# Kernel tuning notes

Hardware: AMD Instinct MI355X
Metric: run time of the kernel (lower is better)

The kernel has to match this reference:

```python
import jax, jax.numpy as jnp
import numpy as np

T, H, E, I = 512, 2048, 8, 1024


def setup_inputs() -> dict:
    key = jax.random.key(0)
    k1, k2, k3, k4 = jax.random.split(key, 4)
    x = jax.random.normal(k1, (T, H), dtype=jnp.float32)
    router_logits = jax.random.normal(k2, (T, E), dtype=jnp.float32)
    # w13 stacks [gate; up] along the output dim: [E, 2I, H]
    w13_weight = jax.random.normal(k3, (E, 2 * I, H), dtype=jnp.float32) * (1.0 / np.sqrt(H))
    w2_weight = jax.random.normal(k4, (E, H, I), dtype=jnp.float32) * (1.0 / np.sqrt(I))
    return {"x": x, "router_logits": router_logits, "w13_weight": w13_weight,
            "w2_weight": w2_weight, "top_k": 2}


def reference(x, router_logits, w13_weight, w2_weight, top_k):
    t, h = x.shape
    e = router_logits.shape[-1]
    # select_experts: softmax -> top_k -> renormalize
    probs = jax.nn.softmax(router_logits.astype(jnp.float32), axis=-1)  # [T, E]
    topk_w, topk_ids = jax.lax.top_k(probs, top_k)                      # [T, K]
    topk_w = topk_w / jnp.sum(topk_w, axis=-1, keepdims=True)
    # dense combine weights [T, E]; zero for unselected experts
    combine = jnp.zeros((t, e), dtype=x.dtype).at[
        jnp.arange(t)[:, None], topk_ids
    ].add(topk_w.astype(x.dtype))
    # grouped expert SwiGLU MLP (computed densely over experts, masked by combine)
    gu = jnp.einsum('th,enh->ten', x, w13_weight)   # [T, E, 2I]
    i = gu.shape[-1] // 2
    gate, up = gu[..., :i], gu[..., i:]
    act = jax.nn.silu(gate) * up                    # [T, E, I]
    y = jnp.einsum('tei,ehi->teh', act, w2_weight)  # [T, E, H]
    return jnp.einsum('teh,te->th', y, combine)     # weighted combine [T, H]
```

## Files before the change

### kernel.cpp

```cpp
#include <hip/hip_runtime.h>
#include <hip/hip_bf16.h>

#define T_TOK 512
#define H_DIM 2048
#define E_NUM 8
#define I_DIM 1024

typedef __attribute__((ext_vector_type(8))) short short8;
typedef __attribute__((ext_vector_type(4))) float f32x4;

__device__ __forceinline__ unsigned short f2bf(float f) {
    unsigned int u = __float_as_uint(f);
    u += 0x7fff + ((u >> 16) & 1);
    return (unsigned short)(u >> 16);
}

__device__ __forceinline__ short8 pack8(float4 a, float4 b) {
    short8 r;
    r[0] = (short)f2bf(a.x); r[1] = (short)f2bf(a.y);
    r[2] = (short)f2bf(a.z); r[3] = (short)f2bf(a.w);
    r[4] = (short)f2bf(b.x); r[5] = (short)f2bf(b.y);
    r[6] = (short)f2bf(b.z); r[7] = (short)f2bf(b.w);
    return r;
}

__device__ __forceinline__ short8 cvt8(float4 a, float4 b) {
    union { short8 s; __hip_bfloat162 h[4]; } u;
    u.h[0] = __float22bfloat162_rn(make_float2(a.x, a.y));
    u.h[1] = __float22bfloat162_rn(make_float2(a.z, a.w));
    u.h[2] = __float22bfloat162_rn(make_float2(b.x, b.y));
    u.h[3] = __float22bfloat162_rn(make_float2(b.z, b.w));
    return u.s;
}

__device__ __forceinline__ void gload_lds16(const float* g, float* l) {
    __builtin_amdgcn_global_load_lds(
        (const __attribute__((address_space(1))) void*)g,
        (__attribute__((address_space(3))) void*)l, 16, 0, 0);
}

__global__ __launch_bounds__(512) void routing_kernel(
    const float* __restrict__ logits,
    int* __restrict__ count, int* __restrict__ bucket,
    float* __restrict__ pair_w)
{
    int t = threadIdx.x;
    if (t < E_NUM) count[t] = 0;
    __syncthreads();

    float p[E_NUM];
    float m = -INFINITY;
#pragma unroll
    for (int e = 0; e < E_NUM; ++e) {
        p[e] = logits[t * E_NUM + e];
        m = fmaxf(m, p[e]);
    }
#pragma unroll
    for (int e = 0; e < E_NUM; ++e) p[e] = expf(p[e] - m);
    int i0 = 0;
#pragma unroll
    for (int e = 1; e < E_NUM; ++e) if (p[e] > p[i0]) i0 = e;
    int i1 = (i0 == 0) ? 1 : 0;
#pragma unroll
    for (int e = 0; e < E_NUM; ++e) if (e != i0 && p[e] > p[i1]) i1 = e;
    float denom = p[i0] + p[i1];
    pair_w[2 * t + 0] = p[i0] / denom;
    pair_w[2 * t + 1] = p[i1] / denom;

    int pos0 = atomicAdd(&count[i0], 1);
    bucket[i0 * T_TOK + pos0] = 2 * t + 0;
    int pos1 = atomicAdd(&count[i1], 1);
    bucket[i1 * T_TOK + pos1] = 2 * t + 1;
}

__global__ __launch_bounds__(256) void gemm1_silu_kernel(
    const float* __restrict__ x, const float* __restrict__ w13,
    const int* __restrict__ count, const int* __restrict__ bucket,
    __hip_bfloat16* __restrict__ act)
{
    const int e   = blockIdx.z;
    const int n_e = count[e];
    const int m0  = blockIdx.y * 64;
    if (m0 >= n_e) return;
    const int n0  = blockIdx.x * 64;

    __shared__ float lds[3 * 64 * 64];
    float* sA = lds;
    float* sG = lds + 4096;
    float* sU = lds + 8192;

    const int tid  = threadIdx.x;
    const int lane = tid & 63;
    const int wid  = tid >> 6;
    const int fr   = lane & 15;
    const int fq   = lane >> 4;
    const int wr   = wid >> 1;
    const int wc   = wid & 1;

    const int lrow = lane >> 4;
    const int slot = lane & 15;

    const float* aptr[4];
    const float* gptr[4];
    const float* uptr[4];
#pragma unroll
    for (int i = 0; i < 4; ++i) {
        int r   = 16 * wid + 4 * i + lrow;
        int gsl = slot ^ (r & 7);
        int arow = min(m0 + r, n_e - 1);
        int tok  = bucket[e * T_TOK + arow] >> 1;
        aptr[i] = x + (size_t)tok * H_DIM + gsl * 4;
        gptr[i] = w13 + ((size_t)e * (2 * I_DIM) + n0 + r) * H_DIM + gsl * 4;
        uptr[i] = w13 + ((size_t)e * (2 * I_DIM) + I_DIM + n0 + r) * H_DIM + gsl * 4;
    }

    f32x4 accg[2][2] = {};
    f32x4 accu[2][2] = {};

#pragma unroll
    for (int i = 0; i < 4; ++i) {
        float* dA = &sA[(16 * wid + 4 * i) * 64];
        float* dG = &sG[(16 * wid + 4 * i) * 64];
        float* dU = &sU[(16 * wid + 4 * i) * 64];
        gload_lds16(aptr[i], dA);
        gload_lds16(gptr[i], dG);
        gload_lds16(uptr[i], dU);
    }

    for (int kb = 64; kb <= H_DIM; kb += 64) {
        __syncthreads();

        short8 a[2][2], bg[2][2], bu[2][2];
#pragma unroll
        for (int kk = 0; kk < 2; ++kk) {
#pragma unroll
            for (int m = 0; m < 2; ++m) {
                int r  = wr * 32 + m * 16 + fr;
                int s0 = (kk * 8 + fq * 2) ^ (r & 7);
                float4 q0 = *(const float4*)&sA[r * 64 + s0 * 4];
                float4 q1 = *(const float4*)&sA[r * 64 + (s0 ^ 1) * 4];
                a[kk][m] = cvt8(q0, q1);
            }
#pragma unroll
            for (int n = 0; n < 2; ++n) {
                int r  = wc * 32 + n * 16 + fr;
                int s0 = (kk * 8 + fq * 2) ^ (r & 7);
                float4 g0 = *(const float4*)&sG[r * 64 + s0 * 4];
                float4 g1 = *(const float4*)&sG[r * 64 + (s0 ^ 1) * 4];
                bg[kk][n] = cvt8(g0, g1);
                float4 u0 = *(const float4*)&sU[r * 64 + s0 * 4];
                float4 u1 = *(const float4*)&sU[r * 64 + (s0 ^ 1) * 4];
                bu[kk][n] = cvt8(u0, u1);
            }
        }
        __syncthreads();

        if (kb < H_DIM) {
#pragma unroll
            for (int i = 0; i < 4; ++i) {
                float* dA = &sA[(16 * wid + 4 * i) * 64];
                float* dG = &sG[(16 * wid + 4 * i) * 64];
                float* dU = &sU[(16 * wid + 4 * i) * 64];
                gload_lds16(aptr[i] + kb, dA);
                gload_lds16(gptr[i] + kb, dG);
                gload_lds16(uptr[i] + kb, dU);
            }
        }

#pragma unroll
        for (int kk = 0; kk < 2; ++kk)
#pragma unroll
            for (int m = 0; m < 2; ++m)
#pragma unroll
                for (int n = 0; n < 2; ++n) {
                    accg[m][n] = __builtin_amdgcn_mfma_f32_16x16x32_bf16(a[kk][m], bg[kk][n], accg[m][n], 0, 0, 0);
                    accu[m][n] = __builtin_amdgcn_mfma_f32_16x16x32_bf16(a[kk][m], bu[kk][n], accu[m][n], 0, 0, 0);
                }
    }

#pragma unroll
    for (int m = 0; m < 2; ++m) {
#pragma unroll
        for (int j = 0; j < 4; ++j) {
            int r = m0 + wr * 32 + m * 16 + fq * 4 + j;
            if (r < n_e) {
                int pid = bucket[e * T_TOK + r];
                __hip_bfloat16* arow = act + (size_t)pid * I_DIM;
#pragma unroll
                for (int n = 0; n < 2; ++n) {
                    float g = accg[m][n][j];
                    float u = accu[m][n][j];
                    float sg = g / (1.f + expf(-g));
                    unsigned short v = f2bf(sg * u);
                    int col = n0 + wc * 32 + n * 16 + fr;
                    *(unsigned short*)(arow + col) = v;
                }
            }
        }
    }
}

__global__ __launch_bounds__(256) void gemm2_kernel(
    const __hip_bfloat16* __restrict__ act, const float* __restrict__ w2,
    const int* __restrict__ count, const int* __restrict__ bucket,
    float* __restrict__ y)
{
    const int e   = blockIdx.z;
    const int n_e = count[e];
    const int m0  = blockIdx.y * 64;
    if (m0 >= n_e) return;
    const int h0  = blockIdx.x * 64;

    __shared__ unsigned short sA[64][72];
    __shared__ unsigned short sB[64][72];

    const int tid = threadIdx.x;
    const int sr = tid >> 2;
    const int sc = (tid & 3) * 16;

    const int rowIdx   = m0 + sr;
    const int pid_load = bucket[e * T_TOK + min(rowIdx, n_e - 1)];
    const __hip_bfloat16* arow = act + (size_t)pid_load * I_DIM;
    const float* brow = w2 + ((size_t)e * H_DIM + (h0 + sr)) * I_DIM;

    const int lane = tid & 63;
    const int wid  = tid >> 6;
    const int wr   = wid >> 1;
    const int wc   = wid & 1;
    const int fr   = lane & 15;
    const int fq   = lane >> 4;

    f32x4 acc[2][2] = {};

    for (int kb = 0; kb < I_DIM; kb += 64) {
        short8 aw0 = *(const short8*)(arow + kb + sc);
        short8 aw1 = *(const short8*)(arow + kb + sc + 8);
        float4 bv0 = *(const float4*)(brow + kb + sc);
        float4 bv1 = *(const float4*)(brow + kb + sc + 4);
        float4 bv2 = *(const float4*)(brow + kb + sc + 8);
        float4 bv3 = *(const float4*)(brow + kb + sc + 12);

        __syncthreads();
        *(short8*)&sA[sr][sc]     = aw0;
        *(short8*)&sA[sr][sc + 8] = aw1;
        *(short8*)&sB[sr][sc]     = pack8(bv0, bv1);
        *(short8*)&sB[sr][sc + 8] = pack8(bv2, bv3);
        __syncthreads();

#pragma unroll
        for (int kk = 0; kk < 2; ++kk) {
            short8 a[2], b[2];
#pragma unroll
            for (int m = 0; m < 2; ++m)
                a[m] = *(const short8*)&sA[wr * 32 + m * 16 + fr][kk * 32 + fq * 8];
#pragma unroll
            for (int n = 0; n < 2; ++n)
                b[n] = *(const short8*)&sB[wc * 32 + n * 16 + fr][kk * 32 + fq * 8];
#pragma unroll
            for (int m = 0; m < 2; ++m)
#pragma unroll
                for (int n = 0; n < 2; ++n)
                    acc[m][n] = __builtin_amdgcn_mfma_f32_16x16x32_bf16(a[m], b[n], acc[m][n], 0, 0, 0);
        }
    }

#pragma unroll
    for (int m = 0; m < 2; ++m) {
#pragma unroll
        for (int j = 0; j < 4; ++j) {
            int r = m0 + wr * 32 + m * 16 + fq * 4 + j;
            if (r < n_e) {
                int pid = bucket[e * T_TOK + r];
                float* yrow = y + (size_t)pid * H_DIM;
#pragma unroll
                for (int n = 0; n < 2; ++n)
                    yrow[h0 + wc * 32 + n * 16 + fr] = acc[m][n][j];
            }
        }
    }
}

__global__ __launch_bounds__(256) void combine_kernel(
    const float* __restrict__ y, const float* __restrict__ pair_w,
    float* __restrict__ out)
{
    int idx = blockIdx.x * 256 + threadIdx.x;
    int t = idx >> 9;
    int c = idx & 511;
    float w0 = pair_w[2 * t + 0];
    float w1 = pair_w[2 * t + 1];
    float4 y0 = ((const float4*)(y + (size_t)(2 * t + 0) * H_DIM))[c];
    float4 y1 = ((const float4*)(y + (size_t)(2 * t + 1) * H_DIM))[c];
    float4 o;
    o.x = w0 * y0.x + w1 * y1.x;
    o.y = w0 * y0.y + w1 * y1.y;
    o.z = w0 * y0.z + w1 * y1.z;
    o.w = w0 * y0.w + w1 * y1.w;
    ((float4*)(out + (size_t)t * H_DIM))[c] = o;
}

extern "C" void kernel_launch(void* const* d_in, const int* in_sizes, int n_in,
                              void* d_out, int out_size, void* d_ws, size_t ws_size,
                              hipStream_t stream) {
    const float* x      = (const float*)d_in[0];
    const float* logits = (const float*)d_in[1];
    const float* w13    = (const float*)d_in[2];
    const float* w2     = (const float*)d_in[3];
    float* out = (float*)d_out;

    int*   count  = (int*)d_ws;
    int*   bucket = count + E_NUM;
    float* pair_w = (float*)(bucket + E_NUM * T_TOK);
    __hip_bfloat16* act = (__hip_bfloat16*)(pair_w + 2 * T_TOK);
    float* ybuf   = (float*)(act + (size_t)2 * T_TOK * I_DIM);

    routing_kernel<<<1, 512, 0, stream>>>(logits, count, bucket, pair_w);
    gemm1_silu_kernel<<<dim3(I_DIM / 64, T_TOK / 64, E_NUM), 256, 0, stream>>>(
        x, w13, count, bucket, act);
    gemm2_kernel<<<dim3(H_DIM / 64, T_TOK / 64, E_NUM), 256, 0, stream>>>(
        act, w2, count, bucket, ybuf);
    combine_kernel<<<(T_TOK * (H_DIM / 4)) / 256, 256, 0, stream>>>(
        ybuf, pair_w, out);
}
```

Baseline: 100.3 us.

## Double-buffer LDS staging with async global-to-LDS loads in both expert GEMMs

Both expert GEMMs now keep two LDS buffers and issue the next tile's global-to-LDS loads before computing the current tile. Explicit vmcnt and lgkmcnt waits with raw barriers replace the __syncthreads pairs. In gemm1 the K tile shrinks to 32 so the double buffer fits in LDS. gemm2 also switches from register-staged loads with pack8 conversion to direct global_load_lds with swizzled fp32 W2 tiles, converting to bf16 at fragment read. The goal is to hide global memory latency behind MFMA work, at the cost of more barrier rounds in gemm1 and reliance on hand-counted vmcnt values.

```diff
diff --git a/kernel.cpp b/kernel.cpp
--- a/kernel.cpp
+++ b/kernel.cpp
@@ -13,15 +13,6 @@
     unsigned int u = __float_as_uint(f);
     u += 0x7fff + ((u >> 16) & 1);
     return (unsigned short)(u >> 16);
-}
-
-__device__ __forceinline__ short8 pack8(float4 a, float4 b) {
-    short8 r;
-    r[0] = (short)f2bf(a.x); r[1] = (short)f2bf(a.y);
-    r[2] = (short)f2bf(a.z); r[3] = (short)f2bf(a.w);
-    r[4] = (short)f2bf(b.x); r[5] = (short)f2bf(b.y);
-    r[6] = (short)f2bf(b.z); r[7] = (short)f2bf(b.w);
-    return r;
 }
 
 __device__ __forceinline__ short8 cvt8(float4 a, float4 b) {
@@ -33,7 +24,7 @@
     return u.s;
 }
 
-__device__ __forceinline__ void gload_lds16(const float* g, float* l) {
+__device__ __forceinline__ void gload_lds16(const void* g, void* l) {
     __builtin_amdgcn_global_load_lds(
         (const __attribute__((address_space(1))) void*)g,
         (__attribute__((address_space(3))) void*)l, 16, 0, 0);
@@ -84,10 +75,7 @@
     if (m0 >= n_e) return;
     const int n0  = blockIdx.x * 64;
 
-    __shared__ float lds[3 * 64 * 64];
-    float* sA = lds;
-    float* sG = lds + 4096;
-    float* sU = lds + 8192;
+    __shared__ float lds[2][3 * 64 * 32];
 
     const int tid  = threadIdx.x;
     const int lane = tid & 63;
@@ -97,86 +85,82 @@
     const int wr   = wid >> 1;
     const int wc   = wid & 1;
 
-    const int lrow = lane >> 4;
-    const int slot = lane & 15;
-
-    const float* aptr[4];
-    const float* gptr[4];
-    const float* uptr[4];
-#pragma unroll
-    for (int i = 0; i < 4; ++i) {
-        int r   = 16 * wid + 4 * i + lrow;
+    const int srow = lane >> 3;
+    const int slot = lane & 7;
+
+    const float *aptr[2], *gptr[2], *uptr[2];
+#pragma unroll
+    for (int ii = 0; ii < 2; ++ii) {
+        int r   = 16 * wid + 8 * ii + srow;
         int gsl = slot ^ (r & 7);
-        int arow = min(m0 + r, n_e - 1);
-        int tok  = bucket[e * T_TOK + arow] >> 1;
-        aptr[i] = x + (size_t)tok * H_DIM + gsl * 4;
-        gptr[i] = w13 + ((size_t)e * (2 * I_DIM) + n0 + r) * H_DIM + gsl * 4;
-        uptr[i] = w13 + ((size_t)e * (2 * I_DIM) + I_DIM + n0 + r) * H_DIM + gsl * 4;
-    }
+        int tok = bucket[e * T_TOK + min(m0 + r, n_e - 1)] >> 1;
+        aptr[ii] = x + (size_t)tok * H_DIM + gsl * 4;
+        gptr[ii] = w13 + ((size_t)e * (2 * I_DIM) + n0 + r) * H_DIM + gsl * 4;
+        uptr[ii] = w13 + ((size_t)e * (2 * I_DIM) + I_DIM + n0 + r) * H_DIM + gsl * 4;
+    }
+
+    auto stage = [&](int kb, int buf) {
+        float* b = lds[buf];
+#pragma unroll
+        for (int ii = 0; ii < 2; ++ii) {
+            int rb = (16 * wid + 8 * ii) * 32;
+            gload_lds16(aptr[ii] + kb, b + rb);
+            gload_lds16(gptr[ii] + kb, b + 2048 + rb);
+            gload_lds16(uptr[ii] + kb, b + 4096 + rb);
+        }
+    };
 
     f32x4 accg[2][2] = {};
     f32x4 accu[2][2] = {};
-
-#pragma unroll
-    for (int i = 0; i < 4; ++i) {
-        float* dA = &sA[(16 * wid + 4 * i) * 64];
-        float* dG = &sG[(16 * wid + 4 * i) * 64];
-        float* dU = &sU[(16 * wid + 4 * i) * 64];
-        gload_lds16(aptr[i], dA);
-        gload_lds16(gptr[i], dG);
-        gload_lds16(uptr[i], dU);
-    }
-
-    for (int kb = 64; kb <= H_DIM; kb += 64) {
-        __syncthreads();
-
-        short8 a[2][2], bg[2][2], bu[2][2];
-#pragma unroll
-        for (int kk = 0; kk < 2; ++kk) {
-#pragma unroll
-            for (int m = 0; m < 2; ++m) {
-                int r  = wr * 32 + m * 16 + fr;
-                int s0 = (kk * 8 + fq * 2) ^ (r & 7);
-                float4 q0 = *(const float4*)&sA[r * 64 + s0 * 4];
-                float4 q1 = *(const float4*)&sA[r * 64 + (s0 ^ 1) * 4];
-                a[kk][m] = cvt8(q0, q1);
-            }
+    short8 a[2], bg[2], bu[2];
+
+    auto readfrags = [&](const float* b) {
+#pragma unroll
+        for (int m = 0; m < 2; ++m) {
+            int r  = wr * 32 + m * 16 + fr;
+            int s0 = (fq * 2) ^ (r & 7);
+            float4 q0 = *(const float4*)(b + r * 32 + s0 * 4);
+            float4 q1 = *(const float4*)(b + r * 32 + (s0 ^ 1) * 4);
+            a[m] = cvt8(q0, q1);
+        }
+#pragma unroll
+        for (int n = 0; n < 2; ++n) {
+            int r  = wc * 32 + n * 16 + fr;
+            int s0 = (fq * 2) ^ (r & 7);
+            float4 g0 = *(const float4*)(b + 2048 + r * 32 + s0 * 4);
+            float4 g1 = *(const float4*)(b + 2048 + r * 32 + (s0 ^ 1) * 4);
+            bg[n] = cvt8(g0, g1);
+            float4 u0 = *(const float4*)(b + 4096 + r * 32 + s0 * 4);
+            float4 u1 = *(const float4*)(b + 4096 + r * 32 + (s0 ^ 1) * 4);
+            bu[n] = cvt8(u0, u1);
+        }
+    };
+
+    auto domfma = [&]() {
+#pragma unroll
+        for (int m = 0; m < 2; ++m)
 #pragma unroll
             for (int n = 0; n < 2; ++n) {
-                int r  = wc * 32 + n * 16 + fr;
-                int s0 = (kk * 8 + fq * 2) ^ (r & 7);
-                float4 g0 = *(const float4*)&sG[r * 64 + s0 * 4];
-                float4 g1 = *(const float4*)&sG[r * 64 + (s0 ^ 1) * 4];
-                bg[kk][n] = cvt8(g0, g1);
-                float4 u0 = *(const float4*)&sU[r * 64 + s0 * 4];
-                float4 u1 = *(const float4*)&sU[r * 64 + (s0 ^ 1) * 4];
-                bu[kk][n] = cvt8(u0, u1);
-            }
-        }
-        __syncthreads();
-
-        if (kb < H_DIM) {
-#pragma unroll
-            for (int i = 0; i < 4; ++i) {
-                float* dA = &sA[(16 * wid + 4 * i) * 64];
-                float* dG = &sG[(16 * wid + 4 * i) * 64];
-                float* dU = &sU[(16 * wid + 4 * i) * 64];
-                gload_lds16(aptr[i] + kb, dA);
-                gload_lds16(gptr[i] + kb, dG);
-                gload_lds16(uptr[i] + kb, dU);
-            }
-        }
-
-#pragma unroll
-        for (int kk = 0; kk < 2; ++kk)
-#pragma unroll
-            for (int m = 0; m < 2; ++m)
-#pragma unroll
-                for (int n = 0; n < 2; ++n) {
-                    accg[m][n] = __builtin_amdgcn_mfma_f32_16x16x32_bf16(a[kk][m], bg[kk][n], accg[m][n], 0, 0, 0);
-                    accu[m][n] = __builtin_amdgcn_mfma_f32_16x16x32_bf16(a[kk][m], bu[kk][n], accu[m][n], 0, 0, 0);
-                }
-    }
+                accg[m][n] = __builtin_amdgcn_mfma_f32_16x16x32_bf16(a[m], bg[n], accg[m][n], 0, 0, 0);
+                accu[m][n] = __builtin_amdgcn_mfma_f32_16x16x32_bf16(a[m], bu[n], accu[m][n], 0, 0, 0);
+            }
+    };
+
+    stage(0, 0);
+#pragma unroll 2
+    for (int t = 0; t < 63; ++t) {
+        stage((t + 1) * 32, (t + 1) & 1);
+        asm volatile("s_waitcnt vmcnt(6)" ::: "memory");
+        __builtin_amdgcn_s_barrier();
+        readfrags(lds[t & 1]);
+        asm volatile("s_waitcnt lgkmcnt(0)" ::: "memory");
+        __builtin_amdgcn_s_barrier();
+        domfma();
+    }
+    asm volatile("s_waitcnt vmcnt(0)" ::: "memory");
+    __builtin_amdgcn_s_barrier();
+    readfrags(lds[1]);
+    domfma();
 
 #pragma unroll
     for (int m = 0; m < 2; ++m) {
@@ -211,58 +195,90 @@
     if (m0 >= n_e) return;
     const int h0  = blockIdx.x * 64;
 
-    __shared__ unsigned short sA[64][72];
-    __shared__ unsigned short sB[64][72];
-
-    const int tid = threadIdx.x;
-    const int sr = tid >> 2;
-    const int sc = (tid & 3) * 16;
-
-    const int rowIdx   = m0 + sr;
-    const int pid_load = bucket[e * T_TOK + min(rowIdx, n_e - 1)];
-    const __hip_bfloat16* arow = act + (size_t)pid_load * I_DIM;
-    const float* brow = w2 + ((size_t)e * H_DIM + (h0 + sr)) * I_DIM;
-
+    __shared__ unsigned short sA[2][64 * 64];
+    __shared__ float sB[2][64 * 64];
+
+    const int tid  = threadIdx.x;
     const int lane = tid & 63;
     const int wid  = tid >> 6;
+    const int fr   = lane & 15;
+    const int fq   = lane >> 4;
     const int wr   = wid >> 1;
     const int wc   = wid & 1;
-    const int fr   = lane & 15;
-    const int fq   = lane >> 4;
+
+    const __hip_bfloat16* a2ptr[2];
+#pragma unroll
+    for (int ii = 0; ii < 2; ++ii) {
+        int r   = 16 * wid + 8 * ii + (lane >> 3);
+        int gsl = (lane & 7) ^ (r & 7);
+        int pid = bucket[e * T_TOK + min(m0 + r, n_e - 1)];
+        a2ptr[ii] = act + (size_t)pid * I_DIM + gsl * 8;
+    }
+    const float* b2ptr[4];
+#pragma unroll
+    for (int i = 0; i < 4; ++i) {
+        int r   = 16 * wid + 4 * i + (lane >> 4);
+        int gsl = (lane & 15) ^ (r & 7);
+        b2ptr[i] = w2 + ((size_t)e * H_DIM + h0 + r) * I_DIM + gsl * 4;
+    }
+
+    auto stage = [&](int kb, int buf) {
+#pragma unroll
+        for (int ii = 0; ii < 2; ++ii)
+            gload_lds16(a2ptr[ii] + kb, &sA[buf][(16 * wid + 8 * ii) * 64]);
+#pragma unroll
+        for (int i = 0; i < 4; ++i)
+            gload_lds16(b2ptr[i] + kb, &sB[buf][(16 * wid + 4 * i) * 64]);
+    };
 
     f32x4 acc[2][2] = {};
-
-    for (int kb = 0; kb < I_DIM; kb += 64) {
-        short8 aw0 = *(const short8*)(arow + kb + sc);
-        short8 aw1 = *(const short8*)(arow + kb + sc + 8);
-        float4 bv0 = *(const float4*)(brow + kb + sc);
-        float4 bv1 = *(const float4*)(brow + kb + sc + 4);
-        float4 bv2 = *(const float4*)(brow + kb + sc + 8);
-        float4 bv3 = *(const float4*)(brow + kb + sc + 12);
-
-        __syncthreads();
-        *(short8*)&sA[sr][sc]     = aw0;
-        *(short8*)&sA[sr][sc + 8] = aw1;
-        *(short8*)&sB[sr][sc]     = pack8(bv0, bv1);
-        *(short8*)&sB[sr][sc + 8] = pack8(bv2, bv3);
-        __syncthreads();
-
+    short8 a[2][2], bf[2][2];
+
+    auto readfrags = [&](int buf) {
 #pragma unroll
         for (int kk = 0; kk < 2; ++kk) {
-            short8 a[2], b[2];
+#pragma unroll
+            for (int m = 0; m < 2; ++m) {
+                int r = wr * 32 + m * 16 + fr;
+                int g = (kk * 4 + fq) ^ (r & 7);
+                a[kk][m] = *(const short8*)&sA[buf][r * 64 + g * 8];
+            }
+#pragma unroll
+            for (int n = 0; n < 2; ++n) {
+                int r  = wc * 32 + n * 16 + fr;
+                int s0 = (kk * 8 + fq * 2) ^ (r & 7);
+                float4 g0 = *(const float4*)&sB[buf][r * 64 + s0 * 4];
+                float4 g1 = *(const float4*)&sB[buf][r * 64 + (s0 ^ 1) * 4];
+                bf[kk][n] = cvt8(g0, g1);
+            }
+        }
+    };
+
+    auto domfma = [&]() {
+#pragma unroll
+        for (int kk = 0; kk < 2; ++kk)
 #pragma unroll
             for (int m = 0; m < 2; ++m)
-                a[m] = *(const short8*)&sA[wr * 32 + m * 16 + fr][kk * 32 + fq * 8];
-#pragma unroll
-            for (int n = 0; n < 2; ++n)
-                b[n] = *(const short8*)&sB[wc * 32 + n * 16 + fr][kk * 32 + fq * 8];
-#pragma unroll
-            for (int m = 0; m < 2; ++m)
 #pragma unroll
                 for (int n = 0; n < 2; ++n)
-                    acc[m][n] = __builtin_amdgcn_mfma_f32_16x16x32_bf16(a[m], b[n], acc[m][n], 0, 0, 0);
-        }
-    }
+                    acc[m][n] = __builtin_amdgcn_mfma_f32_16x16x32_bf16(a[kk][m], bf[kk][n], acc[m][n], 0, 0, 0);
+    };
+
+    stage(0, 0);
+#pragma unroll 2
+    for (int t = 0; t < 15; ++t) {
+        stage((t + 1) * 64, (t + 1) & 1);
+        asm volatile("s_waitcnt vmcnt(6)" ::: "memory");
+        __builtin_amdgcn_s_barrier();
+        readfrags(t & 1);
+        asm volatile("s_waitcnt lgkmcnt(0)" ::: "memory");
+        __builtin_amdgcn_s_barrier();
+        domfma();
+    }
+    asm volatile("s_waitcnt vmcnt(0)" ::: "memory");
+    __builtin_amdgcn_s_barrier();
+    readfrags(1);
+    domfma();
 
 #pragma unroll
     for (int m = 0; m < 2; ++m) {
```

Measured after the change: 95.78 us. -4.5%, faster.
